# Optimization experiments

Measured on AMD Instinct MI355X. Metric: run time of the kernel, lower is better.

## Reference

```python
import jax, jax.numpy as jnp
import numpy as np

DMODEL = 1024
DK = 64
DHEAD = 16
DEPTH = DK * DHEAD
N, LQ, L = 2, 2048, 2048


def setup_inputs() -> dict:
    key = jax.random.key(0)
    ks = jax.random.split(key, 12)
    s = 1.0 / np.sqrt(DMODEL)
    inp = {
        'x': jax.random.normal(ks[0], (N, LQ, DMODEL), jnp.float32),
        'y': jax.random.normal(ks[1], (N, L, DMODEL), jnp.float32),
        'mask': jnp.tril(jnp.ones((LQ, L), dtype=bool)),  # causal
        'Wq': jax.random.normal(ks[2], (DMODEL, DEPTH), jnp.float32) * s,
        'bq': jnp.zeros((DEPTH,), jnp.float32),
        'Wk': jax.random.normal(ks[3], (DMODEL, DEPTH), jnp.float32) * s,
        'bk': jnp.zeros((DEPTH,), jnp.float32),
        'Wv': jax.random.normal(ks[4], (DMODEL, DEPTH), jnp.float32) * s,
        'bv': jnp.zeros((DEPTH,), jnp.float32),
        'Wo': jax.random.normal(ks[5], (DEPTH, DMODEL), jnp.float32) * (1.0 / np.sqrt(DEPTH)),
        'bo': jnp.zeros((DMODEL,), jnp.float32),
    }
    return inp


def reference(x, y, mask, Wq, bq, Wk, bk, Wv, bv, Wo, bo):
    fac = 1.0 / np.sqrt(DK)
    q = (x @ Wq + bq).reshape(N, LQ, DHEAD, DK).transpose(0, 2, 1, 3)  # N,H,Lq,dk
    k = (y @ Wk + bk).reshape(N, L, DHEAD, DK).transpose(0, 2, 1, 3)   # N,H,L,dk
    v = (y @ Wv + bv).reshape(N, L, DHEAD, DK).transpose(0, 2, 1, 3)   # N,H,L,dk
    scores = jnp.einsum('bhqd,bhkd->bhqk', q, k) * fac                 # N,H,Lq,L
    scores = jnp.where(mask, scores, -1e9)  # mask broadcasts over N,H
    attn = jax.nn.softmax(scores, axis=-1)
    out = jnp.einsum('bhqk,bhkd->bhqd', attn, v)                        # N,H,Lq,dk
    out = out.transpose(0, 2, 1, 3).reshape(N, LQ, DEPTH)
    return out @ Wo + bo
```

## Files before the change

kernel.cpp:

```cpp
#include <hip/hip_runtime.h>
#include <hip/hip_bf16.h>

typedef __attribute__((ext_vector_type(8))) short short8;
typedef __attribute__((ext_vector_type(4))) float floatx4;

#define LQ 2048
#define DM 1024
#define NH 16
#define LOG2E 1.44269504088896f

typedef __attribute__((address_space(1))) void gas_t;
typedef __attribute__((address_space(3))) void las_t;

__device__ __forceinline__ void async16(const __hip_bfloat16* g, __hip_bfloat16* l) {
    __builtin_amdgcn_global_load_lds((gas_t*)g, (las_t*)l, 16, 0, 0);
}

__global__ __launch_bounds__(256) void prep_all(
    const float* __restrict__ x,  const float* __restrict__ y,
    const float* __restrict__ Wq, const float* __restrict__ Wk,
    const float* __restrict__ Wv, const float* __restrict__ Wo,
    __hip_bfloat16* __restrict__ xb,  __hip_bfloat16* __restrict__ yb,
    __hip_bfloat16* __restrict__ Wqt, __hip_bfloat16* __restrict__ Wkt,
    __hip_bfloat16* __restrict__ Wvt, __hip_bfloat16* __restrict__ Wot)
{
    __shared__ float tile[64][65];
    const int t  = threadIdx.x;
    const int bx = blockIdx.x;

    if (bx < 4096) {
        const float* in = (bx < 2048) ? x : y;
        __hip_bfloat16* out = (bx < 2048) ? xb : yb;
        const int i = ((bx & 2047) * 256 + t) * 8;
        float4 a0 = ((const float4*)(in + i))[0];
        float4 a1 = ((const float4*)(in + i))[1];
        union { __hip_bfloat16 h[8]; uint4 u; } pk;
        pk.h[0] = __float2bfloat16(a0.x); pk.h[1] = __float2bfloat16(a0.y);
        pk.h[2] = __float2bfloat16(a0.z); pk.h[3] = __float2bfloat16(a0.w);
        pk.h[4] = __float2bfloat16(a1.x); pk.h[5] = __float2bfloat16(a1.y);
        pk.h[6] = __float2bfloat16(a1.z); pk.h[7] = __float2bfloat16(a1.w);
        *(uint4*)(out + i) = pk.u;
        return;
    }

    const int r    = bx - 4096;
    const int wsel = r >> 8;
    const int tid  = r & 255;
    const int n0   = (tid & 15) * 64, k0 = (tid >> 4) * 64;
    const float* W = (wsel == 0) ? Wq : (wsel == 1) ? Wk : (wsel == 2) ? Wv : Wo;
    __hip_bfloat16* Wt = (wsel == 0) ? Wqt : (wsel == 1) ? Wkt : (wsel == 2) ? Wvt : Wot;

    const int rr0 = t >> 4, c4 = (t & 15) * 4;
#pragma unroll
    for (int rr = 0; rr < 64; rr += 16) {
        float4 v = *(const float4*)&W[(size_t)(k0 + rr0 + rr) * DM + n0 + c4];
        tile[rr0 + rr][c4 + 0] = v.x; tile[rr0 + rr][c4 + 1] = v.y;
        tile[rr0 + rr][c4 + 2] = v.z; tile[rr0 + rr][c4 + 3] = v.w;
    }
    __syncthreads();
    const int nr = t >> 2, kc = (t & 3) * 16;
    union { __hip_bfloat16 h[16]; uint4 u[2]; } pk;
#pragma unroll
    for (int i = 0; i < 16; ++i) pk.h[i] = __float2bfloat16(tile[kc + i][nr]);
    uint4* dst = (uint4*)&Wt[(size_t)(n0 + nr) * DM + k0 + kc];
    dst[0] = pk.u[0];
    dst[1] = pk.u[1];
}

__global__ __launch_bounds__(512) void gemm_qkv(
    const __hip_bfloat16* __restrict__ xb,
    const __hip_bfloat16* __restrict__ yb,
    const __hip_bfloat16* __restrict__ Bt,
    const float* __restrict__ bq, const float* __restrict__ bk,
    const float* __restrict__ bv,
    __hip_bfloat16* __restrict__ Qb, __hip_bfloat16* __restrict__ Kb,
    __hip_bfloat16* __restrict__ Vt,
    float qscl)
{
    constexpr int BM = 256, BN = 256, BK = 32, Kd = 1024, NIT = Kd / BK;
    __shared__ __align__(16) __hip_bfloat16 As[3][BM * BK];
    __shared__ __align__(16) __hip_bfloat16 Bs[3][BN * BK];

    const int t    = threadIdx.x;
    const int w    = t >> 6;
    const int lane = t & 63;
    const int quad = lane >> 4;
    const int l16  = lane & 15;
    const int wm   = w & 1;
    const int wn   = w >> 1;

    const int f  = blockIdx.x;
    const int rx = f & 7;
    const int rr = f >> 3;
    const int bx = (rx & 1) * 6 + rr % 6;
    const int by = (rx >> 1) * 4 + rr / 6;
    const int m0 = by * BM;
    const int n0 = bx * BN;

    const int region = n0 >> 10;
    const int nl     = n0 & 1023;

    const __hip_bfloat16* A = (region == 0) ? xb : yb;

    const int lrow = lane >> 2;
    const int lcol = (lane & 3) * 8;

    floatx4 acc[8][4];
#pragma unroll
    for (int i = 0; i < 8; ++i)
#pragma unroll
        for (int j = 0; j < 4; ++j) acc[i][j] = (floatx4){0.f, 0.f, 0.f, 0.f};

    auto stage = [&](int k0, int buf) {
#pragma unroll
        for (int s = 0; s < 2; ++s) {
            const int seg = w * 2 + s;
            async16(A + (size_t)(m0 + seg * 16 + lrow) * Kd + k0 + lcol,
                    &As[buf][seg * 16 * BK]);
            async16(Bt + (size_t)(n0 + seg * 16 + lrow) * Kd + k0 + lcol,
                    &Bs[buf][seg * 16 * BK]);
        }
    };

    stage(0, 0);
    stage(BK, 1);
    int cur = 0;
    for (int i = 0; i < NIT; ++i) {
        if (i < NIT - 1) asm volatile("s_waitcnt vmcnt(4)" ::: "memory");
        else             asm volatile("s_waitcnt vmcnt(0)" ::: "memory");
        __builtin_amdgcn_sched_barrier(0);
        __builtin_amdgcn_s_barrier();
        if (i + 2 < NIT) stage((i + 2) * BK, (cur + 2 >= 3) ? cur - 1 : cur + 2);

        short8 af[8], bf[4];
#pragma unroll
        for (int mi = 0; mi < 8; ++mi)
            af[mi] = *(const short8*)&As[cur][(wm * 128 + mi * 16 + l16) * BK + quad * 8];
#pragma unroll
        for (int j = 0; j < 4; ++j)
            bf[j] = *(const short8*)&Bs[cur][(wn * 64 + j * 16 + l16) * BK + quad * 8];
#pragma unroll
        for (int mi = 0; mi < 8; ++mi)
#pragma unroll
            for (int j = 0; j < 4; ++j)
                acc[mi][j] = __builtin_amdgcn_mfma_f32_16x16x32_bf16(af[mi], bf[j], acc[mi][j], 0, 0, 0);
        cur = (cur + 1 >= 3) ? 0 : cur + 1;
    }

    if (region < 2) {
        __hip_bfloat16* C    = (region == 0) ? Qb : Kb;
        const float*    bias = (region == 0) ? bq : bk;
        const float     scl  = (region == 0) ? qscl : 1.0f;
#pragma unroll
        for (int j = 0; j < 4; ++j) {
            const int col = nl + wn * 64 + j * 16 + l16;
            const float bvv = bias[col];
#pragma unroll
            for (int mi = 0; mi < 8; ++mi) {
#pragma unroll
                for (int r = 0; r < 4; ++r) {
                    const int row = m0 + wm * 128 + mi * 16 + quad * 4 + r;
                    C[(size_t)row * 1024 + col] = __float2bfloat16((acc[mi][j][r] + bvv) * scl);
                }
            }
        }
    } else {
#pragma unroll
        for (int j = 0; j < 4; ++j) {
            const int col = nl + wn * 64 + j * 16 + l16;
            const float bvv = bv[col];
#pragma unroll
            for (int mi = 0; mi < 8; ++mi) {
                const int row0 = m0 + wm * 128 + mi * 16 + quad * 4;
                union { __hip_bfloat16 h4[4]; uint2 u; } pk;
#pragma unroll
                for (int r = 0; r < 4; ++r)
                    pk.h4[r] = __float2bfloat16(acc[mi][j][r] + bvv);
                *(uint2*)&Vt[((size_t)((row0 >> 11) * 1024 + col)) * 2048 + (row0 & 2047)] = pk.u;
            }
        }
    }
}

__global__ __launch_bounds__(256) void gemm_o(
    const __hip_bfloat16* __restrict__ A,
    const __hip_bfloat16* __restrict__ Bt,
    const float* __restrict__ bias,
    float* __restrict__ C,
    int M)
{
    constexpr int BM = 64, BN = 128, BK = 32, Kd = 1024, NIT = Kd / BK;
    __shared__ __align__(16) __hip_bfloat16 As[3][BM * BK];
    __shared__ __align__(16) __hip_bfloat16 Bs[3][BN * BK];

    const int t    = threadIdx.x;
    const int w    = t >> 6;
    const int lane = t & 63;
    const int quad = lane >> 4;
    const int l16  = lane & 15;
    const int wm   = w & 1;
    const int wn   = w >> 1;

    const int f  = blockIdx.x;
    const int rx = f & 7;
    const int rr = f >> 3;
    const int bx = (rx & 1) * 4 + (rr & 3);
    const int by = (rx >> 1) * 16 + (rr >> 2);
    const int m0 = by * BM;
    const int n0 = bx * BN;

    const int lrow = lane >> 2;
    const int lcol = (lane & 3) * 8;

    floatx4 acc[2][4];
#pragma unroll
    for (int i = 0; i < 2; ++i)
#pragma unroll
        for (int j = 0; j < 4; ++j) acc[i][j] = (floatx4){0.f, 0.f, 0.f, 0.f};

    auto stage = [&](int k0, int buf) {
#pragma unroll
        for (int s = 0; s < 3; ++s) {
            const int seg = w * 3 + s;
            if (seg < 4) {
                async16(A + (size_t)(m0 + seg * 16 + lrow) * Kd + k0 + lcol,
                        &As[buf][seg * 16 * BK]);
            } else {
                const int bs = seg - 4;
                async16(Bt + (size_t)(n0 + bs * 16 + lrow) * Kd + k0 + lcol,
                        &Bs[buf][bs * 16 * BK]);
            }
        }
    };

    stage(0, 0);
    stage(BK, 1);
    int cur = 0;
    for (int i = 0; i < NIT; ++i) {
        if (i < NIT - 1) asm volatile("s_waitcnt vmcnt(3)" ::: "memory");
        else             asm volatile("s_waitcnt vmcnt(0)" ::: "memory");
        __builtin_amdgcn_sched_barrier(0);
        __builtin_amdgcn_s_barrier();
        if (i + 2 < NIT) stage((i + 2) * BK, (cur + 2 >= 3) ? cur - 1 : cur + 2);

        short8 af[2], bf[4];
#pragma unroll
        for (int ii = 0; ii < 2; ++ii)
            af[ii] = *(const short8*)&As[cur][(wm * 32 + ii * 16 + l16) * BK + quad * 8];
#pragma unroll
        for (int j = 0; j < 4; ++j)
            bf[j] = *(const short8*)&Bs[cur][(wn * 64 + j * 16 + l16) * BK + quad * 8];
#pragma unroll
        for (int ii = 0; ii < 2; ++ii)
#pragma unroll
            for (int j = 0; j < 4; ++j)
                acc[ii][j] = __builtin_amdgcn_mfma_f32_16x16x32_bf16(af[ii], bf[j], acc[ii][j], 0, 0, 0);
        cur = (cur + 1 >= 3) ? 0 : cur + 1;
    }

#pragma unroll
    for (int j = 0; j < 4; ++j) {
        const int col = n0 + wn * 64 + j * 16 + l16;
        const float bvf = bias[col];
#pragma unroll
        for (int i = 0; i < 2; ++i) {
#pragma unroll
            for (int r = 0; r < 4; ++r) {
                const int row = m0 + wm * 32 + i * 16 + quad * 4 + r;
                C[(size_t)row * 1024 + col] = acc[i][j][r] + bvf;
            }
        }
    }
}

template <bool A_IS_F32, bool OUT_F32, bool TRANSV = false>
__global__ __launch_bounds__(256) void gemm64(
    const void* __restrict__ Av,
    const float* __restrict__ B,
    const float* __restrict__ bias,
    void* __restrict__ Cv,
    int M, int N, int K, float scale)
{
    __shared__ __align__(16) __hip_bfloat16 As[64][40];
    __shared__ __align__(16) __hip_bfloat16 Bs[64][40];

    const int t    = threadIdx.x;
    const int wave = t >> 6;
    const int lane = t & 63;
    const int quad = lane >> 4;
    const int l16  = lane & 15;
    const int m0   = blockIdx.y * 64;
    const int n0   = blockIdx.x * 64;

    floatx4 acc[4];
#pragma unroll
    for (int i = 0; i < 4; ++i) acc[i] = (floatx4){0.f, 0.f, 0.f, 0.f};

    const int arow = t >> 2, acol = (t & 3) * 8;
    const int bkk  = t >> 3, bnn  = (t & 7) * 8;

    for (int k0 = 0; k0 < K; k0 += 32) {
        if constexpr (A_IS_F32) {
            const float* A = (const float*)Av;
            const float* ap = A + (size_t)(m0 + arow) * K + k0 + acol;
            float4 a0 = ((const float4*)ap)[0];
            float4 a1 = ((const float4*)ap)[1];
            union { __hip_bfloat16 h[8]; short8 s; } up;
            up.h[0] = __float2bfloat16(a0.x); up.h[1] = __float2bfloat16(a0.y);
            up.h[2] = __float2bfloat16(a0.z); up.h[3] = __float2bfloat16(a0.w);
            up.h[4] = __float2bfloat16(a1.x); up.h[5] = __float2bfloat16(a1.y);
            up.h[6] = __float2bfloat16(a1.z); up.h[7] = __float2bfloat16(a1.w);
            *(short8*)(&As[arow][acol]) = up.s;
        } else {
            const __hip_bfloat16* A = (const __hip_bfloat16*)Av;
            uint4 av = *(const uint4*)(A + (size_t)(m0 + arow) * K + k0 + acol);
            *(uint4*)(&As[arow][acol]) = av;
        }
        {
            const float* bp = B + (size_t)(k0 + bkk) * N + n0 + bnn;
            float4 b0 = ((const float4*)bp)[0];
            float4 b1 = ((const float4*)bp)[1];
            Bs[bnn + 0][bkk] = __float2bfloat16(b0.x);
            Bs[bnn + 1][bkk] = __float2bfloat16(b0.y);
            Bs[bnn + 2][bkk] = __float2bfloat16(b0.z);
            Bs[bnn + 3][bkk] = __float2bfloat16(b0.w);
            Bs[bnn + 4][bkk] = __float2bfloat16(b1.x);
            Bs[bnn + 5][bkk] = __float2bfloat16(b1.y);
            Bs[bnn + 6][bkk] = __float2bfloat16(b1.z);
            Bs[bnn + 7][bkk] = __float2bfloat16(b1.w);
        }
        __syncthreads();

        short8 afrag = *(const short8*)(&As[wave * 16 + l16][quad * 8]);
#pragma unroll
        for (int nt = 0; nt < 4; ++nt) {
            short8 bfrag = *(const short8*)(&Bs[nt * 16 + l16][quad * 8]);
            acc[nt] = __builtin_amdgcn_mfma_f32_16x16x32_bf16(afrag, bfrag, acc[nt], 0, 0, 0);
        }
        __syncthreads();
    }

#pragma unroll
    for (int nt = 0; nt < 4; ++nt) {
        const int col = n0 + nt * 16 + l16;
        const float bvf = bias[col];
        if constexpr (TRANSV) {
            const int row0 = m0 + wave * 16 + quad * 4;
            union { __hip_bfloat16 h4[4]; uint2 u; } pk;
#pragma unroll
            for (int r = 0; r < 4; ++r)
                pk.h4[r] = __float2bfloat16(acc[nt][r] + bvf);
            *(uint2*)&((__hip_bfloat16*)Cv)[((size_t)((row0 >> 11) * 1024 + col)) * 2048 + (row0 & 2047)] = pk.u;
        } else {
#pragma unroll
            for (int r = 0; r < 4; ++r) {
                const int row = m0 + wave * 16 + quad * 4 + r;
                const float v = (acc[nt][r] + bvf) * scale;
                if constexpr (OUT_F32) ((float*)Cv)[(size_t)row * N + col] = v;
                else ((__hip_bfloat16*)Cv)[(size_t)row * N + col] = __float2bfloat16(v);
            }
        }
    }
}

#define PP 72

__global__ __launch_bounds__(256, 2) void attn_mfma10(
    const __hip_bfloat16* __restrict__ Q,
    const __hip_bfloat16* __restrict__ K,
    const __hip_bfloat16* __restrict__ Vt,
    __hip_bfloat16* __restrict__ O)
{
    __shared__ __align__(16) __hip_bfloat16 KtS[3][64 * 64];
    __shared__ __align__(16) __hip_bfloat16 VtS[3][64 * 64];
    __shared__ __align__(16) __hip_bfloat16 PsQ[128 * PP];

    const int t    = threadIdx.x;
    const int w    = t >> 6;
    const int lane = t & 63;
    const int quad = lane >> 4;
    const int l16  = lane & 15;

    const int f   = blockIdx.x;
    const int xcd = f & 7;
    const int u   = f >> 3;
    const int pi  = u >> 4;
    const int qr  = u & 15;
    const int qx  = (pi & 2) ? (15 - qr) : qr;
    const int p   = xcd * 4 + pi;
    const int h   = p & 15;
    const int b   = p >> 4;
    const int q0  = qx * 128;

    const size_t rowbase = (size_t)b * LQ;
    const int    hcol    = h * 64;
    const size_t vbase   = (size_t)(b * NH + h) * 64 * LQ;

    const int r8 = l16 & 7;

    auto stage = [&](int j0n, int buf) {
#pragma unroll
        for (int rnd = 0; rnd < 2; ++rnd) {
            const int c   = rnd * 256 + t;
            const int row = c >> 3;
            const int ch  = (c & 7) ^ (row & 7);
            async16(K + (rowbase + j0n + row) * DM + hcol + ch * 8,
                    &KtS[buf][c * 8]);
            async16(Vt + vbase + (size_t)row * LQ + j0n + ch * 8,
                    &VtS[buf][c * 8]);
        }
    };

    {
        const int qrow = t >> 1, qseg = (t & 1) * 32;
        const uint4* src = (const uint4*)(Q + (rowbase + q0 + qrow) * DM + hcol + qseg);
        uint4* dst = (uint4*)&PsQ[qrow * PP + qseg];
        dst[0] = src[0]; dst[1] = src[1]; dst[2] = src[2]; dst[3] = src[3];
    }
    stage(0, 0);
    stage(64, 1);

    short8 qf[2][2];
#pragma unroll
    for (int g = 0; g < 2; ++g)
#pragma unroll
        for (int hh = 0; hh < 2; ++hh)
            qf[g][hh] = *(const short8*)&PsQ[(w * 32 + g * 16 + l16) * PP + hh * 32 + quad * 8];

    __hip_bfloat16* Pw = &PsQ[(w * 32) * PP];

    float l_i[2] = {0.f, 0.f};
    floatx4 o[2][4];
#pragma unroll
    for (int g = 0; g < 2; ++g)
#pragma unroll
        for (int i = 0; i < 4; ++i) o[g][i] = (floatx4){0.f, 0.f, 0.f, 0.f};

    const int wq_lo  = q0 + w * 32;
    const int wq_hi  = wq_lo + 31;
    const int ntiles = 2 * qx + 2;

    int cur = 0;
    for (int jt = 0; jt < ntiles; ++jt) {
        const int j0 = jt * 64;

        if (jt < ntiles - 1) asm volatile("s_waitcnt vmcnt(4)" ::: "memory");
        else                 asm volatile("s_waitcnt vmcnt(0)" ::: "memory");
        __builtin_amdgcn_sched_barrier(0);
        __builtin_amdgcn_s_barrier();
        if (jt + 2 < ntiles) stage(j0 + 128, (cur + 2 >= 3) ? cur - 1 : cur + 2);

        if (j0 <= wq_hi) {
            const bool bnd = (j0 + 63 > wq_lo);
#pragma unroll
            for (int jc = 0; jc < 4; ++jc) {
                const __hip_bfloat16* kr = &KtS[cur][(jc * 16 + l16) * 64];
                short8 ak0 = *(const short8*)&kr[((quad    ) ^ r8) * 8];
                short8 ak1 = *(const short8*)&kr[((quad + 4) ^ r8) * 8];
#pragma unroll
                for (int g = 0; g < 2; ++g) {
                    floatx4 z = (floatx4){0.f, 0.f, 0.f, 0.f};
                    z = __builtin_amdgcn_mfma_f32_16x16x32_bf16(ak0, qf[g][0], z, 0, 0, 0);
                    z = __builtin_amdgcn_mfma_f32_16x16x32_bf16(ak1, qf[g][1], z, 0, 0, 0);
                    if (bnd) {
                        const int qg = wq_lo + g * 16 + l16;
#pragma unroll
                        for (int r = 0; r < 4; ++r) {
                            const int j = j0 + jc * 16 + quad * 4 + r;
                            if (j > qg) z[r] = -1e30f;
                        }
                    }
                    union { __hip_bfloat16 h4[4]; uint2 u; } pk;
#pragma unroll
                    for (int r = 0; r < 4; ++r) {
                        const float e = __builtin_amdgcn_exp2f(z[r]);
                        l_i[g] += e;
                        pk.h4[r] = __float2bfloat16(e);
                    }
                    *(uint2*)&Pw[(g * 16 + l16) * PP + jc * 16 + quad * 4] = pk.u;
                }
            }
            short8 pa[2][2];
#pragma unroll
            for (int g = 0; g < 2; ++g) {
                pa[g][0] = *(const short8*)&Pw[(g * 16 + l16) * PP + quad * 8];
                pa[g][1] = *(const short8*)&Pw[(g * 16 + l16) * PP + 32 + quad * 8];
            }
            __builtin_amdgcn_s_setprio(1);
#pragma unroll
            for (int subf = 0; subf < 4; ++subf) {
                const __hip_bfloat16* vr = &VtS[cur][(subf * 16 + l16) * 64];
                short8 vb0 = *(const short8*)&vr[((quad    ) ^ r8) * 8];
                short8 vb1 = *(const short8*)&vr[((quad + 4) ^ r8) * 8];
#pragma unroll
                for (int g = 0; g < 2; ++g) {
                    o[g][subf] = __builtin_amdgcn_mfma_f32_16x16x32_bf16(pa[g][0], vb0, o[g][subf], 0, 0, 0);
                    o[g][subf] = __builtin_amdgcn_mfma_f32_16x16x32_bf16(pa[g][1], vb1, o[g][subf], 0, 0, 0);
                }
            }
            __builtin_amdgcn_s_setprio(0);
        }
        cur = (cur + 1 >= 3) ? 0 : cur + 1;
    }

#pragma unroll
    for (int g = 0; g < 2; ++g) {
        l_i[g] += __shfl_xor(l_i[g], 16);
        l_i[g] += __shfl_xor(l_i[g], 32);
#pragma unroll
        for (int r = 0; r < 4; ++r) {
            const float linv = 1.0f / __shfl(l_i[g], quad * 4 + r);
            const size_t row = rowbase + q0 + w * 32 + g * 16 + quad * 4 + r;
#pragma unroll
            for (int subf = 0; subf < 4; ++subf)
                O[row * DM + hcol + subf * 16 + l16] = __float2bfloat16(o[g][subf][r] * linv);
        }
    }
}

extern "C" void kernel_launch(void* const* d_in, const int* in_sizes, int n_in,
                              void* d_out, int out_size, void* d_ws, size_t ws_size,
                              hipStream_t stream)
{
    (void)in_sizes; (void)n_in; (void)out_size;

    const float* x  = (const float*)d_in[0];
    const float* y  = (const float*)d_in[1];
    const float* Wq = (const float*)d_in[3];
    const float* bq = (const float*)d_in[4];
    const float* Wk = (const float*)d_in[5];
    const float* bk = (const float*)d_in[6];
    const float* Wv = (const float*)d_in[7];
    const float* bv = (const float*)d_in[8];
    const float* Wo = (const float*)d_in[9];
    const float* bo = (const float*)d_in[10];

    const size_t NTOK = (size_t)2 * LQ * DM;
    const size_t MM   = (size_t)DM * DM;
    const int    M    = 2 * LQ;
    const float  QSCL = 0.125f * LOG2E;

    __hip_bfloat16* Qb  = (__hip_bfloat16*)d_ws;
    __hip_bfloat16* Kb  = Qb + NTOK;
    __hip_bfloat16* Vtb = Kb + NTOK;
    __hip_bfloat16* Ab  = Vtb + NTOK;

    const size_t need = (4 * NTOK + 2 * NTOK + 4 * MM) * sizeof(__hip_bfloat16);
    const dim3 agrid(512, 1, 1);

    if (ws_size >= need) {
        __hip_bfloat16* xb  = Ab + NTOK;
        __hip_bfloat16* yb  = xb + NTOK;
        __hip_bfloat16* Wqt = yb + NTOK;
        __hip_bfloat16* Wkt = Wqt + MM;
        __hip_bfloat16* Wvt = Wkt + MM;
        __hip_bfloat16* Wot = Wvt + MM;
        (void)Wkt; (void)Wvt;

        prep_all<<<5120, 256, 0, stream>>>(x, y, Wq, Wk, Wv, Wo,
                                           xb, yb, Wqt, Wkt, Wvt, Wot);

        gemm_qkv<<<192, 512, 0, stream>>>(xb, yb, Wqt, bq, bk, bv, Qb, Kb, Vtb, QSCL);
        attn_mfma10<<<agrid, 256, 0, stream>>>(Qb, Kb, Vtb, Ab);
        gemm_o<<<512, 256, 0, stream>>>(Ab, Wot, bo, (float*)d_out, M);
    } else {
        const dim3 gblk(DM / 64, M / 64);
        gemm64<true,  false><<<gblk, 256, 0, stream>>>(x, Wq, bq, Qb, M, DM, DM, QSCL);
        gemm64<true,  false><<<gblk, 256, 0, stream>>>(y, Wk, bk, Kb, M, DM, DM, 1.0f);
        gemm64<true,  false, true><<<gblk, 256, 0, stream>>>(y, Wv, bv, Vtb, M, DM, DM, 1.0f);
        attn_mfma10<<<agrid, 256, 0, stream>>>(Qb, Kb, Vtb, Ab);
        gemm64<false, true ><<<gblk, 256, 0, stream>>>(Ab, Wo, bo, (float*)d_out, M, DM, DM, 1.0f);
    }
}
```

Measured before the change: 227.3 us.

## Restructure QKV GEMM mainloop with 4-slot buffering, XOR swizzle, and split-phase MFMA

The QKV projection GEMM mainloop now uses four LDS slots instead of three. It applies an XOR swizzle on the 16-byte chunk index to cut LDS bank conflicts on fragment reads. Each k-step is split into two halves, with A and B prefetches issued separately between the MFMA batches, and the MFMA sections are wrapped in s_setprio raised priority. The aim is better overlap of global-to-LDS loads, LDS reads and matrix math. The cost is extra barriers per iteration and more LDS use.

```diff
diff --git a/kernel.cpp b/kernel.cpp
--- a/kernel.cpp
+++ b/kernel.cpp
@@ -77,9 +77,10 @@
     __hip_bfloat16* __restrict__ Vt,
     float qscl)
 {
-    constexpr int BM = 256, BN = 256, BK = 32, Kd = 1024, NIT = Kd / BK;
-    __shared__ __align__(16) __hip_bfloat16 As[3][BM * BK];
-    __shared__ __align__(16) __hip_bfloat16 Bs[3][BN * BK];
+    constexpr int BM = 256, BN = 256, Kd = 1024;
+    constexpr int NHS = Kd / 32;
+    __shared__ __align__(16) __hip_bfloat16 As[4][256 * 32];
+    __shared__ __align__(16) __hip_bfloat16 Bs[4][256 * 32];
 
     const int t    = threadIdx.x;
     const int w    = t >> 6;
@@ -102,49 +103,89 @@
 
     const __hip_bfloat16* A = (region == 0) ? xb : yb;
 
-    const int lrow = lane >> 2;
-    const int lcol = (lane & 3) * 8;
-
     floatx4 acc[8][4];
 #pragma unroll
     for (int i = 0; i < 8; ++i)
 #pragma unroll
         for (int j = 0; j < 4; ++j) acc[i][j] = (floatx4){0.f, 0.f, 0.f, 0.f};
 
-    auto stage = [&](int k0, int buf) {
-#pragma unroll
-        for (int s = 0; s < 2; ++s) {
-            const int seg = w * 2 + s;
-            async16(A + (size_t)(m0 + seg * 16 + lrow) * Kd + k0 + lcol,
-                    &As[buf][seg * 16 * BK]);
-            async16(Bt + (size_t)(n0 + seg * 16 + lrow) * Kd + k0 + lcol,
-                    &Bs[buf][seg * 16 * BK]);
+    auto stageA = [&](int h) {
+        const int k0 = h * 32, slot = h & 3;
+#pragma unroll
+        for (int l = 0; l < 2; ++l) {
+            const int c   = l * 512 + t;
+            const int row = c >> 2;
+            const int ch  = (c & 3) ^ ((row >> 1) & 3);
+            async16(A + (size_t)(m0 + row) * Kd + k0 + ch * 8, &As[slot][c * 8]);
         }
     };
-
-    stage(0, 0);
-    stage(BK, 1);
-    int cur = 0;
-    for (int i = 0; i < NIT; ++i) {
-        if (i < NIT - 1) asm volatile("s_waitcnt vmcnt(4)" ::: "memory");
-        else             asm volatile("s_waitcnt vmcnt(0)" ::: "memory");
+    auto stageB = [&](int h) {
+        const int k0 = h * 32, slot = h & 3;
+#pragma unroll
+        for (int l = 0; l < 2; ++l) {
+            const int c   = l * 512 + t;
+            const int row = c >> 2;
+            const int ch  = (c & 3) ^ ((row >> 1) & 3);
+            async16(Bt + (size_t)(n0 + row) * Kd + k0 + ch * 8, &Bs[slot][c * 8]);
+        }
+    };
+
+    stageA(0); stageB(0); stageA(1); stageB(1);
+    asm volatile("s_waitcnt vmcnt(4)" ::: "memory");
+    __builtin_amdgcn_sched_barrier(0);
+    __builtin_amdgcn_s_barrier();
+
+    const int csw = (l16 >> 1) & 3;
+
+    for (int h = 0; h < NHS; ++h) {
+        const int slot = h & 3;
+        const __hip_bfloat16* as = &As[slot][0];
+        const __hip_bfloat16* bs = &Bs[slot][0];
+        short8 af[8], bf[4];
+
+#pragma unroll
+        for (int nj = 0; nj < 4; ++nj) {
+            const int row = wn * 64 + nj * 16 + l16;
+            bf[nj] = *(const short8*)&bs[row * 32 + (quad ^ csw) * 8];
+        }
+#pragma unroll
+        for (int mi = 0; mi < 4; ++mi) {
+            const int row = wm * 128 + mi * 16 + l16;
+            af[mi] = *(const short8*)&as[row * 32 + (quad ^ csw) * 8];
+        }
+        if (h + 2 < NHS) stageA(h + 2);
+        __builtin_amdgcn_s_barrier();
+        asm volatile("s_waitcnt lgkmcnt(0)" ::: "memory");
+        __builtin_amdgcn_sched_barrier(0);
+        __builtin_amdgcn_s_setprio(1);
+#pragma unroll
+        for (int mi = 0; mi < 4; ++mi)
+#pragma unroll
+            for (int nj = 0; nj < 4; ++nj)
+                acc[mi][nj] = __builtin_amdgcn_mfma_f32_16x16x32_bf16(af[mi], bf[nj], acc[mi][nj], 0, 0, 0);
+        __builtin_amdgcn_s_setprio(0);
+        __builtin_amdgcn_s_barrier();
+
+#pragma unroll
+        for (int mi = 4; mi < 8; ++mi) {
+            const int row = wm * 128 + mi * 16 + l16;
+            af[mi] = *(const short8*)&as[row * 32 + (quad ^ csw) * 8];
+        }
+        if (h + 2 < NHS) stageB(h + 2);
+        __builtin_amdgcn_s_barrier();
+        asm volatile("s_waitcnt lgkmcnt(0)" ::: "memory");
+        __builtin_amdgcn_sched_barrier(0);
+        __builtin_amdgcn_s_setprio(1);
+#pragma unroll
+        for (int mi = 4; mi < 8; ++mi)
+#pragma unroll
+            for (int nj = 0; nj < 4; ++nj)
+                acc[mi][nj] = __builtin_amdgcn_mfma_f32_16x16x32_bf16(af[mi], bf[nj], acc[mi][nj], 0, 0, 0);
+        __builtin_amdgcn_s_setprio(0);
+        if (h + 2 < NHS)      asm volatile("s_waitcnt vmcnt(4)" ::: "memory");
+        else                  asm volatile("s_waitcnt vmcnt(0)" ::: "memory");
         __builtin_amdgcn_sched_barrier(0);
         __builtin_amdgcn_s_barrier();
-        if (i + 2 < NIT) stage((i + 2) * BK, (cur + 2 >= 3) ? cur - 1 : cur + 2);
-
-        short8 af[8], bf[4];
-#pragma unroll
-        for (int mi = 0; mi < 8; ++mi)
-            af[mi] = *(const short8*)&As[cur][(wm * 128 + mi * 16 + l16) * BK + quad * 8];
-#pragma unroll
-        for (int j = 0; j < 4; ++j)
-            bf[j] = *(const short8*)&Bs[cur][(wn * 64 + j * 16 + l16) * BK + quad * 8];
-#pragma unroll
-        for (int mi = 0; mi < 8; ++mi)
-#pragma unroll
-            for (int j = 0; j < 4; ++j)
-                acc[mi][j] = __builtin_amdgcn_mfma_f32_16x16x32_bf16(af[mi], bf[j], acc[mi][j], 0, 0, 0);
-        cur = (cur + 1 >= 3) ? 0 : cur + 1;
     }
 
     if (region < 2) {
```

Measured after the change: 216.8 us. 1.05x faster.
